# Optimization experiments

Measured on AMD Instinct MI355X. Metric: run time of the kernel, lower is better.

## Reference

```python
import jax, jax.numpy as jnp
import numpy as np

B, S, D = 4, 2048, 1024   # batch, seq_len, input feature dim
H, E = 16, 64             # head_num, att_embedding_size; H*E = model dim


def setup_inputs() -> dict:
    key = jax.random.key(0)
    ks = jax.random.split(key, 9)
    std = 1.0 / np.sqrt(D)
    M = H * E
    return {
        "x": jax.random.normal(ks[0], (B, S, D), dtype=jnp.float32),
        "Wq": jax.random.normal(ks[1], (D, M), dtype=jnp.float32) * std,
        "bq": jnp.zeros((M,), dtype=jnp.float32),
        "Wk": jax.random.normal(ks[2], (D, M), dtype=jnp.float32) * std,
        "bk": jnp.zeros((M,), dtype=jnp.float32),
        "Wv": jax.random.normal(ks[3], (D, M), dtype=jnp.float32) * std,
        "bv": jnp.zeros((M,), dtype=jnp.float32),
        "Wr": jax.random.normal(ks[4], (D, M), dtype=jnp.float32) * std,
        "br": jnp.zeros((M,), dtype=jnp.float32),
    }


def reference(x, Wq, bq, Wk, bk, Wv, bv, Wr, br):
    # QKV dense layers with ReLU activation (as in the original Keras code)
    qw = jax.nn.relu(x @ Wq + bq)                      # [B,S,H*E]
    kw = jax.nn.relu(x @ Wk + bk)
    vw = jax.nn.relu(x @ Wv + bv)
    # split heads: [B,S,H,E] -> [B,H,S,E]
    qw = qw.reshape(B, S, H, E).transpose(0, 2, 1, 3)
    kw = kw.reshape(B, S, H, E).transpose(0, 2, 1, 3)
    vw = vw.reshape(B, S, H, E).transpose(0, 2, 1, 3)
    # unscaled attention (original has no 1/sqrt(d) scaling)
    a = jnp.einsum("bhqe,bhke->bhqk", qw, kw)          # [B,H,S,S]
    a = jax.nn.softmax(a, axis=-1)
    o = jnp.einsum("bhqk,bhke->bhqe", a, vw)           # [B,H,S,E]
    o = o.transpose(0, 2, 1, 3).reshape(B, S, H * E)
    # residual dense (no activation)
    o = o + (x @ Wr + br)
    return o
```

## Files before the change

### kernel.cpp

```cpp
#include <hip/hip_runtime.h>


typedef __bf16 bf16x8 __attribute__((ext_vector_type(8)));
typedef float  f32x4  __attribute__((ext_vector_type(4)));
typedef short  short8 __attribute__((ext_vector_type(8)));
typedef short  short4v __attribute__((ext_vector_type(4)));
typedef float  float4v __attribute__((ext_vector_type(4)));
typedef int    int4v  __attribute__((ext_vector_type(4)));
typedef unsigned uint2v __attribute__((ext_vector_type(2)));

#define LOG2E 1.44269504088896f

__device__ __forceinline__ unsigned short f2bf(float f) {
  unsigned u = __builtin_bit_cast(unsigned, f);
  u += 0x7fffu + ((u >> 16) & 1u);
  return (unsigned short)(u >> 16);
}

__device__ __forceinline__ unsigned pack2(float lo, float hi) {
  __bf16 a = (__bf16)lo, b = (__bf16)hi;
  unsigned short ua = __builtin_bit_cast(unsigned short, a);
  unsigned short ub = __builtin_bit_cast(unsigned short, b);
  return (unsigned)ua | ((unsigned)ub << 16);
}

__global__ __launch_bounds__(256) void k_cvt_x(const float* __restrict__ x,
                                               short* __restrict__ Xb) {
  const size_t i = ((size_t)blockIdx.x * 256 + threadIdx.x) * 4;
  float4v f = *(const float4v*)(x + i);
  short4v o;
  o[0] = (short)f2bf(f[0]); o[1] = (short)f2bf(f[1]);
  o[2] = (short)f2bf(f[2]); o[3] = (short)f2bf(f[3]);
  *(short4v*)(Xb + i) = o;
}

__global__ __launch_bounds__(256) void k_cvt_w(const float* __restrict__ Wq,
                                               const float* __restrict__ Wk,
                                               const float* __restrict__ Wv,
                                               const float* __restrict__ Wr,
                                               short* __restrict__ Wc) {
  const int bid = blockIdx.x;
  const int w = bid >> 8;
  const int t = bid & 255;
  const int tr = t >> 4, tc = t & 15;
  const float* Ws = (w == 0) ? Wq : (w == 1) ? Wk : (w == 2) ? Wv : Wr;
  __shared__ float T[64][65];
  const int tx = threadIdx.x & 63, ty = threadIdx.x >> 6;
#pragma unroll
  for (int i = 0; i < 16; ++i)
    T[i * 4 + ty][tx] = Ws[(size_t)(tr * 64 + i * 4 + ty) * 1024 + tc * 64 + tx];
  __syncthreads();
#pragma unroll
  for (int i = 0; i < 16; ++i) {
    const int n = tc * 64 + i * 4 + ty;
    Wc[((size_t)w * 1024 + n) * 1024 + tr * 64 + tx] = (short)f2bf(T[tx][i * 4 + ty]);
  }
}

__global__ __launch_bounds__(512, 2) void k_gemm(const short* __restrict__ Xb,
                                                 const short* __restrict__ Wc,
                                                 const float* __restrict__ bq,
                                                 const float* __restrict__ bk2,
                                                 const float* __restrict__ bv,
                                                 const float* __restrict__ br,
                                                 short* __restrict__ Qb,
                                                 short* __restrict__ Kb,
                                                 short* __restrict__ Vt,
                                                 float* __restrict__ Out) {
  __shared__ __align__(16) short smem[65536];
  char* const sb = (char*)smem;
  const int tid = threadIdx.x, wid = tid >> 6, lane = tid & 63;
  const int lr = lane & 15, hi = lane >> 4;
  const int bm = blockIdx.x & 31, bn = blockIdx.x >> 5;
  const int m0 = bm * 256, n0 = bn * 256;
  const int wm = wid >> 2, wn = wid & 3;

  f32x4 acc[8][4] = {};

  const int sl_ = (tid & 7) ^ ((tid >> 3) & 7);
  const int rA0 = ((tid >> 3) << 1) + (sl_ >> 2);
  const short* sa0 = Xb + (size_t)(m0 + rA0) * 1024 + (sl_ & 3) * 8;
  const short* sa1 = Xb + (size_t)(m0 + 128 + rA0) * 1024 + (sl_ & 3) * 8;
  const short* sg0 = Wc + (size_t)(n0 + rA0) * 1024 + (sl_ & 3) * 8;
  const short* sg1 = Wc + (size_t)(n0 + 128 + rA0) * 1024 + (sl_ & 3) * 8;

  const int xr = (((lane & 1) * 4 + hi) ^ ((lr >> 1) & 7)) * 16;
  const int amb = wm * 8192 + (lr >> 1) * 128 + xr;
  const int bnb = 65536 + wn * 4096 + (lr >> 1) * 128 + xr;

#define GLL(SRC, LDSOFF)                                                                   \
  __builtin_amdgcn_global_load_lds((const __attribute__((address_space(1))) void*)(SRC),   \
      (__attribute__((address_space(3))) void*)(sb + (LDSOFF)), 16, 0, 0)

#define STAGE(SLOT)                                                                        \
  do {                                                                                     \
    GLL(sa0, (SLOT) * 16384 + wid * 1024);                                                 \
    GLL(sa1, (SLOT) * 16384 + 8192 + wid * 1024);                                          \
    GLL(sg0, 65536 + (SLOT) * 16384 + wid * 1024);                                         \
    GLL(sg1, 65536 + (SLOT) * 16384 + 8192 + wid * 1024);                                  \
    sa0 += 32; sa1 += 32; sg0 += 32; sg1 += 32;                                            \
  } while (0)

#define PHASE(J, VM, STG)                                                                  \
  do {                                                                                     \
    asm volatile("s_waitcnt vmcnt(" #VM ")" ::: "memory");                                 \
    __builtin_amdgcn_sched_barrier(0);                                                     \
    __builtin_amdgcn_s_barrier();                                                          \
    __builtin_amdgcn_sched_barrier(0);                                                     \
    if (STG) STAGE(((J) + 3) & 3);                                                         \
    bf16x8 am[8], bnr[4];                                                                  \
    _Pragma("unroll")                                                                      \
    for (int mf = 0; mf < 8; ++mf)                                                         \
      am[mf] = *(const bf16x8*)(sb + (((J) & 3) * 16384 + amb + mf * 1024));               \
    _Pragma("unroll")                                                                      \
    for (int nf = 0; nf < 4; ++nf)                                                         \
      bnr[nf] = *(const bf16x8*)(sb + (((J) & 3) * 16384 + bnb + nf * 1024));              \
    asm volatile("s_waitcnt lgkmcnt(0)" ::: "memory");                                     \
    __builtin_amdgcn_sched_barrier(0);                                                     \
    __builtin_amdgcn_s_setprio(1);                                                         \
    _Pragma("unroll")                                                                      \
    for (int mf = 0; mf < 8; ++mf)                                                         \
      _Pragma("unroll")                                                                    \
      for (int nf = 0; nf < 4; ++nf)                                                       \
        acc[mf][nf] = __builtin_amdgcn_mfma_f32_16x16x32_bf16(am[mf], bnr[nf],             \
                                                              acc[mf][nf], 0, 0, 0);      \
    __builtin_amdgcn_s_setprio(0);                                                         \
    __builtin_amdgcn_sched_barrier(0);                                                     \
  } while (0)

  STAGE(0);
  STAGE(1);
  STAGE(2);

  for (int it = 0; it < 7; ++it) {
    PHASE(0, 8, 1);
    PHASE(1, 8, 1);
    PHASE(2, 8, 1);
    PHASE(3, 8, 1);
  }
  PHASE(0, 8, 1);
  PHASE(1, 8, 0);
  PHASE(2, 4, 0);
  PHASE(3, 0, 0);
#undef PHASE
#undef STAGE
#undef GLL

#pragma unroll
  for (int mf = 0; mf < 8; ++mf) {
    const int mbase = m0 + wm * 128 + mf * 16 + hi * 4;
    const int bb2 = mbase >> 11, sbase = mbase & 2047;
#pragma unroll
    for (int nf = 0; nf < 4; ++nf) {
      const int n = n0 + wn * 64 + nf * 16 + lr;
      const float* bp = (n < 2048) ? (n < 1024 ? bq : bk2) : (n < 3072 ? bv : br);
      const float bias = bp[n & 1023];
      float v[4];
#pragma unroll
      for (int r = 0; r < 4; ++r) v[r] = acc[mf][nf][r] + bias;

      if (n < 2048) {
        const int nn = n & 1023, h = nn >> 6, e = nn & 63;
        short* dst = (n < 1024) ? Qb : Kb;
        const float scale = (n < 1024) ? LOG2E : 1.0f;
#pragma unroll
        for (int r = 0; r < 4; ++r)
          dst[(((size_t)bb2 * 16 + h) * 2048 + sbase + r) * 64 + e] =
              (short)f2bf(fmaxf(v[r], 0.f) * scale);
      } else if (n < 3072) {
        const int nn = n & 1023, h = nn >> 6, e = nn & 63;
        const int kq = sbase & 31;
        const int Sp = (sbase & ~31) + ((kq >> 2) & 3) * 8 + (kq >> 4) * 4;
        uint2v pv;
        pv[0] = pack2(fmaxf(v[0], 0.f), fmaxf(v[1], 0.f));
        pv[1] = pack2(fmaxf(v[2], 0.f), fmaxf(v[3], 0.f));
        *(uint2v*)&Vt[(((size_t)bb2 * 16 + h) * 64 + e) * 2048 + Sp] = pv;
      } else {
#pragma unroll
        for (int r = 0; r < 4; ++r)
          Out[(size_t)(mbase + r) * 1024 + (n - 3072)] = v[r];
      }
    }
  }
}

__global__ __launch_bounds__(256, 4) void k_attn(const short* __restrict__ Qb,
                                                 const short* __restrict__ Kb,
                                                 const short* __restrict__ Vt,
                                                 float* __restrict__ Out) {
  __shared__ __align__(16) short smem[16384];
  char* const sb = (char*)smem;
  const int tid = threadIdx.x, wid = tid >> 6, lane = tid & 63;
  const int lr = lane & 15, hi = lane >> 4;
  const int bid = ((blockIdx.x & 7) << 7) | (blockIdx.x >> 3);
  const int bh = bid >> 4;
  const int q0 = (bid & 15) * 128;
  const size_t hb = (size_t)bh * (2048 * 64);

  bf16x8 aq[2][2];
#pragma unroll
  for (int g = 0; g < 2; ++g) {
    const short* qp = Qb + hb + (size_t)(q0 + wid * 32 + g * 16 + lr) * 64 + hi * 8;
    aq[g][0] = *(const bf16x8*)qp;
    aq[g][1] = *(const bf16x8*)(qp + 32);
  }

  f32x4 o[2][4] = {};
  float l_run[2] = {0.f, 0.f};

  const int swz = ((lane & 7) ^ (lane >> 3)) * 8;
  const int rlo = lane >> 3;
  const int wr0 = wid * 16;
  const short* kp0 = Kb + hb + (size_t)(wr0 + rlo) * 64 + swz;
  const short* kp1 = kp0 + 8 * 64;
  const short* vp0 = Vt + hb + (size_t)(wr0 + rlo) * 2048 + swz;
  const short* vp1 = vp0 + 8 * 2048;

  const int vb0 = (lr * 64 + ((hi ^ (lr & 7)) << 3)) * 2;
  const int vb1 = vb0 ^ 64;

#define GLL(SRC, LDSOFF)                                                                   \
  __builtin_amdgcn_global_load_lds((const __attribute__((address_space(1))) void*)(SRC),   \
      (__attribute__((address_space(3))) void*)(sb + (LDSOFF)), 16, 0, 0)

  GLL(kp0, wr0 * 128);
  GLL(kp1, wr0 * 128 + 1024);
  GLL(vp0, 16384 + wr0 * 128);
  GLL(vp1, 16384 + wr0 * 128 + 1024);
  kp0 += 4096; kp1 += 4096; vp0 += 64; vp1 += 64;
  __syncthreads();

  for (int kt = 0; kt < 32; ++kt) {
    const int buf = kt & 1;
    if (kt < 31) {
      const int d = (buf ^ 1) * 8192 + wr0 * 128;
      GLL(kp0, d);
      GLL(kp1, d + 1024);
      GLL(vp0, 16384 + d);
      GLL(vp1, 16384 + d + 1024);
      kp0 += 4096; kp1 += 4096; vp0 += 64; vp1 += 64;
    }

    f32x4 s[2][4];
    __builtin_amdgcn_s_setprio(1);
#pragma unroll
    for (int kc = 0; kc < 4; ++kc) {
      const bf16x8 kf0 = *(const bf16x8*)(sb + (vb0 + buf * 8192 + kc * 2048));
      const bf16x8 kf1 = *(const bf16x8*)(sb + (vb1 + buf * 8192 + kc * 2048));
      f32x4 t0 = __builtin_amdgcn_mfma_f32_16x16x32_bf16(kf0, aq[0][0], (f32x4){0.f, 0.f, 0.f, 0.f}, 0, 0, 0);
      s[0][kc] = __builtin_amdgcn_mfma_f32_16x16x32_bf16(kf1, aq[0][1], t0, 0, 0, 0);
      f32x4 t1 = __builtin_amdgcn_mfma_f32_16x16x32_bf16(kf0, aq[1][0], (f32x4){0.f, 0.f, 0.f, 0.f}, 0, 0, 0);
      s[1][kc] = __builtin_amdgcn_mfma_f32_16x16x32_bf16(kf1, aq[1][1], t1, 0, 0, 0);
    }
    __builtin_amdgcn_s_setprio(0);

    int4v pw[2][2];
#pragma unroll
    for (int g = 0; g < 2; ++g) {
      float sum = 0.f;
#pragma unroll
      for (int kc = 0; kc < 4; ++kc) {
        const float p0 = __builtin_amdgcn_exp2f(s[g][kc][0]);
        const float p1 = __builtin_amdgcn_exp2f(s[g][kc][1]);
        const float p2 = __builtin_amdgcn_exp2f(s[g][kc][2]);
        const float p3 = __builtin_amdgcn_exp2f(s[g][kc][3]);
        sum += (p0 + p1) + (p2 + p3);
        pw[g][kc >> 1][(kc & 1) * 2] = (int)pack2(p0, p1);
        pw[g][kc >> 1][(kc & 1) * 2 + 1] = (int)pack2(p2, p3);
      }
      l_run[g] += sum;
    }

    __builtin_amdgcn_s_setprio(1);
#pragma unroll
    for (int kk = 0; kk < 2; ++kk) {
      const bf16x8 pa0 = __builtin_bit_cast(bf16x8, pw[0][kk]);
      const bf16x8 pa1 = __builtin_bit_cast(bf16x8, pw[1][kk]);
      const int cb = (kk ? vb1 : vb0) + 16384 + buf * 8192;
#pragma unroll
      for (int et = 0; et < 4; ++et) {
        const bf16x8 vf = *(const bf16x8*)(sb + (cb + et * 2048));
        o[0][et] = __builtin_amdgcn_mfma_f32_16x16x32_bf16(vf, pa0, o[0][et], 0, 0, 0);
        o[1][et] = __builtin_amdgcn_mfma_f32_16x16x32_bf16(vf, pa1, o[1][et], 0, 0, 0);
      }
    }
    __builtin_amdgcn_s_setprio(0);

    __syncthreads();
  }

  float* Ep = (float*)smem + wid * 1088;
  const int b = bh >> 4, h = bh & 15;
  const int qr = lane >> 2, cc = lane & 3;
#pragma unroll
  for (int g = 0; g < 2; ++g) {
    float lt = l_run[g];
    lt += __shfl_xor(lt, 16);
    lt += __shfl_xor(lt, 32);
    const float inv = 1.0f / lt;
#pragma unroll
    for (int et = 0; et < 4; ++et) {
      f32x4 v = o[g][et] * inv;
      *(float4v*)&Ep[lr * 68 + et * 16 + hi * 4] = v;
    }
    asm volatile("s_waitcnt lgkmcnt(0)" ::: "memory");
    const size_t gb = ((size_t)b * 2048 + q0 + wid * 32 + g * 16 + qr) * 1024 + h * 64 + cc * 4;
#pragma unroll
    for (int i = 0; i < 4; ++i) {
      float4v v = *(const float4v*)&Ep[qr * 68 + cc * 4 + i * 16];
      float4v u = *(const float4v*)&Out[gb + i * 16];
      u += v;
      *(float4v*)&Out[gb + i * 16] = u;
    }
    asm volatile("s_waitcnt lgkmcnt(0)" ::: "memory");
  }
#undef GLL
}

extern "C" void kernel_launch(void* const* d_in, const int* in_sizes, int n_in,
                              void* d_out, int out_size, void* d_ws, size_t ws_size,
                              hipStream_t stream) {
  const float* x  = (const float*)d_in[0];
  const float* Wq = (const float*)d_in[1];
  const float* bq = (const float*)d_in[2];
  const float* Wk = (const float*)d_in[3];
  const float* bk = (const float*)d_in[4];
  const float* Wv = (const float*)d_in[5];
  const float* bv = (const float*)d_in[6];
  const float* Wr = (const float*)d_in[7];
  const float* br = (const float*)d_in[8];
  float* Out = (float*)d_out;

  char* ws = (char*)d_ws;
  short* Xb = (short*)(ws);
  short* Wc = (short*)(ws + (size_t)16 * 1024 * 1024);
  short* Qb = (short*)(ws + (size_t)24 * 1024 * 1024);
  short* Kb = (short*)(ws + (size_t)40 * 1024 * 1024);
  short* Vt = (short*)(ws + (size_t)56 * 1024 * 1024);

  k_cvt_x<<<8192, 256, 0, stream>>>(x, Xb);
  k_cvt_w<<<1024, 256, 0, stream>>>(Wq, Wk, Wv, Wr, Wc);
  k_gemm<<<512, 512, 0, stream>>>(Xb, Wc, bq, bk, bv, br, Qb, Kb, Vt, Out);
  k_attn<<<1024, 256, 0, stream>>>(Qb, Kb, Vt, Out);
}
```

Before: 166.5 us.

## Merge conversion kernels and stage Q/K epilogue through LDS for coalesced stores

The x and weight fp32-to-bf16 conversion kernels become a single launch that dispatches on block index, saving one kernel launch. In the GEMM epilogue, Q and K outputs are first written to a per-wave LDS tile and then stored to global memory as 16-byte vectors along the head dimension, replacing scattered 2-byte stores. The epilogue branches are also specialised per wave on the column base. This adds a block barrier and LDS traffic after the main loop in exchange for wider, coalesced global writes.

```diff
diff --git a/kernel.cpp b/kernel.cpp
--- a/kernel.cpp
+++ b/kernel.cpp
@@ -24,36 +24,37 @@
   return (unsigned)ua | ((unsigned)ub << 16);
 }
 
-__global__ __launch_bounds__(256) void k_cvt_x(const float* __restrict__ x,
-                                               short* __restrict__ Xb) {
-  const size_t i = ((size_t)blockIdx.x * 256 + threadIdx.x) * 4;
-  float4v f = *(const float4v*)(x + i);
-  short4v o;
-  o[0] = (short)f2bf(f[0]); o[1] = (short)f2bf(f[1]);
-  o[2] = (short)f2bf(f[2]); o[3] = (short)f2bf(f[3]);
-  *(short4v*)(Xb + i) = o;
-}
-
-__global__ __launch_bounds__(256) void k_cvt_w(const float* __restrict__ Wq,
-                                               const float* __restrict__ Wk,
-                                               const float* __restrict__ Wv,
-                                               const float* __restrict__ Wr,
-                                               short* __restrict__ Wc) {
+__global__ __launch_bounds__(256) void k_cvt(const float* __restrict__ x,
+                                             const float* __restrict__ Wq,
+                                             const float* __restrict__ Wk,
+                                             const float* __restrict__ Wv,
+                                             const float* __restrict__ Wr,
+                                             short* __restrict__ Xb,
+                                             short* __restrict__ Wc) {
+  __shared__ float T[64][65];
   const int bid = blockIdx.x;
-  const int w = bid >> 8;
-  const int t = bid & 255;
-  const int tr = t >> 4, tc = t & 15;
-  const float* Ws = (w == 0) ? Wq : (w == 1) ? Wk : (w == 2) ? Wv : Wr;
-  __shared__ float T[64][65];
-  const int tx = threadIdx.x & 63, ty = threadIdx.x >> 6;
-#pragma unroll
-  for (int i = 0; i < 16; ++i)
-    T[i * 4 + ty][tx] = Ws[(size_t)(tr * 64 + i * 4 + ty) * 1024 + tc * 64 + tx];
-  __syncthreads();
-#pragma unroll
-  for (int i = 0; i < 16; ++i) {
-    const int n = tc * 64 + i * 4 + ty;
-    Wc[((size_t)w * 1024 + n) * 1024 + tr * 64 + tx] = (short)f2bf(T[tx][i * 4 + ty]);
+  if (bid < 8192) {
+    const size_t i = ((size_t)bid * 256 + threadIdx.x) * 4;
+    float4v f = *(const float4v*)(x + i);
+    short4v o;
+    o[0] = (short)f2bf(f[0]); o[1] = (short)f2bf(f[1]);
+    o[2] = (short)f2bf(f[2]); o[3] = (short)f2bf(f[3]);
+    *(short4v*)(Xb + i) = o;
+  } else {
+    const int t = (bid - 8192) & 255;
+    const int w = (bid - 8192) >> 8;
+    const int tr = t >> 4, tc = t & 15;
+    const float* Ws = (w == 0) ? Wq : (w == 1) ? Wk : (w == 2) ? Wv : Wr;
+    const int tx = threadIdx.x & 63, ty = threadIdx.x >> 6;
+#pragma unroll
+    for (int i = 0; i < 16; ++i)
+      T[i * 4 + ty][tx] = Ws[(size_t)(tr * 64 + i * 4 + ty) * 1024 + tc * 64 + tx];
+    __syncthreads();
+#pragma unroll
+    for (int i = 0; i < 16; ++i) {
+      const int n = tc * 64 + i * 4 + ty;
+      Wc[((size_t)w * 1024 + n) * 1024 + tr * 64 + tx] = (short)f2bf(T[tx][i * 4 + ty]);
+    }
   }
 }
 
@@ -146,39 +147,66 @@
 #undef STAGE
 #undef GLL
 
-#pragma unroll
-  for (int mf = 0; mf < 8; ++mf) {
-    const int mbase = m0 + wm * 128 + mf * 16 + hi * 4;
-    const int bb2 = mbase >> 11, sbase = mbase & 2047;
-#pragma unroll
-    for (int nf = 0; nf < 4; ++nf) {
-      const int n = n0 + wn * 64 + nf * 16 + lr;
-      const float* bp = (n < 2048) ? (n < 1024 ? bq : bk2) : (n < 3072 ? bv : br);
-      const float bias = bp[n & 1023];
-      float v[4];
-#pragma unroll
-      for (int r = 0; r < 4; ++r) v[r] = acc[mf][nf][r] + bias;
-
-      if (n < 2048) {
-        const int nn = n & 1023, h = nn >> 6, e = nn & 63;
-        short* dst = (n < 1024) ? Qb : Kb;
-        const float scale = (n < 1024) ? LOG2E : 1.0f;
+  __syncthreads();
+
+  const int nbase = n0 + wn * 64;
+  if (nbase < 2048) {
+    short* dst = (nbase < 1024) ? Qb : Kb;
+    const float scale = (nbase < 1024) ? LOG2E : 1.0f;
+    const float* bp = (nbase < 1024) ? bq : bk2;
+    const int h = (nbase & 1023) >> 6;
+    float bias[4];
+#pragma unroll
+    for (int nf = 0; nf < 4; ++nf) bias[nf] = bp[(nbase & 1023) + nf * 16 + lr];
+    short* Wl = smem + wid * 1152;
+    const int srow = lane >> 2, sc = lane & 3;
+#pragma unroll
+    for (int mf = 0; mf < 8; ++mf) {
+#pragma unroll
+      for (int nf = 0; nf < 4; ++nf)
 #pragma unroll
         for (int r = 0; r < 4; ++r)
-          dst[(((size_t)bb2 * 16 + h) * 2048 + sbase + r) * 64 + e] =
-              (short)f2bf(fmaxf(v[r], 0.f) * scale);
-      } else if (n < 3072) {
-        const int nn = n & 1023, h = nn >> 6, e = nn & 63;
+          Wl[(hi * 4 + r) * 72 + nf * 16 + lr] =
+              (short)f2bf(fmaxf(acc[mf][nf][r] + bias[nf], 0.f) * scale);
+      asm volatile("s_waitcnt lgkmcnt(0)" ::: "memory");
+      const int mbase = m0 + wm * 128 + mf * 16;
+      const int bb2 = mbase >> 11, sb2 = mbase & 2047;
+      short8 v0 = *(const short8*)&Wl[srow * 72 + sc * 16];
+      short8 v1 = *(const short8*)&Wl[srow * 72 + sc * 16 + 8];
+      short* gp = dst + (((size_t)bb2 * 16 + h) * 2048 + sb2 + srow) * 64 + sc * 16;
+      *(short8*)gp = v0;
+      *(short8*)(gp + 8) = v1;
+      asm volatile("s_waitcnt lgkmcnt(0)" ::: "memory");
+    }
+  } else if (nbase < 3072) {
+#pragma unroll
+    for (int mf = 0; mf < 8; ++mf) {
+      const int mbase = m0 + wm * 128 + mf * 16 + hi * 4;
+      const int bb2 = mbase >> 11, sbase = mbase & 2047;
+#pragma unroll
+      for (int nf = 0; nf < 4; ++nf) {
+        const int n = nbase + nf * 16 + lr;
+        const float bias = bv[n & 1023];
+        const int nn = n & 1023, h2 = nn >> 6, e = nn & 63;
         const int kq = sbase & 31;
         const int Sp = (sbase & ~31) + ((kq >> 2) & 3) * 8 + (kq >> 4) * 4;
         uint2v pv;
-        pv[0] = pack2(fmaxf(v[0], 0.f), fmaxf(v[1], 0.f));
-        pv[1] = pack2(fmaxf(v[2], 0.f), fmaxf(v[3], 0.f));
-        *(uint2v*)&Vt[(((size_t)bb2 * 16 + h) * 64 + e) * 2048 + Sp] = pv;
-      } else {
+        pv[0] = pack2(fmaxf(acc[mf][nf][0] + bias, 0.f), fmaxf(acc[mf][nf][1] + bias, 0.f));
+        pv[1] = pack2(fmaxf(acc[mf][nf][2] + bias, 0.f), fmaxf(acc[mf][nf][3] + bias, 0.f));
+        *(uint2v*)&Vt[(((size_t)bb2 * 16 + h2) * 64 + e) * 2048 + Sp] = pv;
+      }
+    }
+  } else {
+#pragma unroll
+    for (int mf = 0; mf < 8; ++mf) {
+      const int mbase = m0 + wm * 128 + mf * 16 + hi * 4;
+#pragma unroll
+      for (int nf = 0; nf < 4; ++nf) {
+        const int n = nbase + nf * 16 + lr;
+        const float bias = br[n & 1023];
 #pragma unroll
         for (int r = 0; r < 4; ++r)
-          Out[(size_t)(mbase + r) * 1024 + (n - 3072)] = v[r];
+          Out[(size_t)(mbase + r) * 1024 + (n - 3072)] = acc[mf][nf][r] + bias;
       }
     }
   }
@@ -338,8 +366,7 @@
   short* Kb = (short*)(ws + (size_t)40 * 1024 * 1024);
   short* Vt = (short*)(ws + (size_t)56 * 1024 * 1024);
 
-  k_cvt_x<<<8192, 256, 0, stream>>>(x, Xb);
-  k_cvt_w<<<1024, 256, 0, stream>>>(Wq, Wk, Wv, Wr, Wc);
+  k_cvt<<<9216, 256, 0, stream>>>(x, Wq, Wk, Wv, Wr, Xb, Wc);
   k_gemm<<<512, 512, 0, stream>>>(Xb, Wc, bq, bk, bv, br, Qb, Kb, Vt, Out);
   k_attn<<<1024, 256, 0, stream>>>(Qb, Kb, Vt, Out);
 }
```

Result: no change. 165.3 us (-0.7%).
